# Optimization experiments

Hardware: AMD Instinct MI355X
Metric: run time of the kernel (lower is better)

The kernel has to match this reference:

```python
import jax, jax.numpy as jnp
import numpy as np

XZ = jnp.array([0, 2])
XY = jnp.array([0, 1])
YZ = jnp.array([1, 2])


def _bilinear(plane, uv):
    """plane: (C,R,R) as (C,H,W); uv: (N,2) in [0,1], uv[:,0]->width, uv[:,1]->height.
    Border padding + align_corners=True semantics (grid_sample style)."""
    R = plane.shape[-1]
    xy = jnp.clip(uv, 0.0, 1.0) * (R - 1)
    x, y = xy[:, 0], xy[:, 1]
    x0 = jnp.floor(x)
    y0 = jnp.floor(y)
    x0i = jnp.clip(x0.astype(jnp.int32), 0, R - 1)
    y0i = jnp.clip(y0.astype(jnp.int32), 0, R - 1)
    x1i = jnp.clip(x0i + 1, 0, R - 1)
    y1i = jnp.clip(y0i + 1, 0, R - 1)
    wx = (x - x0)[None, :]  # (1,N)
    wy = (y - y0)[None, :]
    f00 = plane[:, y0i, x0i]  # (C,N)
    f01 = plane[:, y0i, x1i]
    f10 = plane[:, y1i, x0i]
    f11 = plane[:, y1i, x1i]
    top = f00 * (1.0 - wx) + f01 * wx
    bot = f10 * (1.0 - wx) + f11 * wx
    return (top * (1.0 - wy) + bot * wy).T  # (N,C)


def _sample_triplane(p, c_xz, c_xy, c_yz):
    """p: (bs,N,3) in [0,1]; planes: (bs,C,R,R). Returns (bs,N,C) summed over planes."""
    def per_batch(pb, fxz, fxy, fyz):
        return (_bilinear(fxz, pb[:, XZ])
                + _bilinear(fxy, pb[:, XY])
                + _bilinear(fyz, pb[:, YZ]))
    return jax.vmap(per_batch)(p, c_xz, c_xy, c_yz)


def setup_inputs() -> dict:
    key = jax.random.key(0)
    ks = jax.random.split(key, 12)
    bs, ns, C, S, R = 2, 50000, 32, 8, 128
    inp = {
        "query_pos": jax.random.uniform(ks[0], (bs, ns, 3), dtype=jnp.float32),
        "c_xz": jax.random.normal(ks[1], (bs, C, R, R), dtype=jnp.float32),
        "c_xy": jax.random.normal(ks[2], (bs, C, R, R), dtype=jnp.float32),
        "c_yz": jax.random.normal(ks[3], (bs, C, R, R), dtype=jnp.float32),
        # offset weights scaled small so sampled points stay mostly in-bounds
        "W_off": jax.random.normal(ks[4], (C, S * 3), dtype=jnp.float32) * 0.01,
        "b_off": jnp.zeros((S * 3,), dtype=jnp.float32),
        "W_w": jax.random.normal(ks[5], (C, S), dtype=jnp.float32) * 0.1,
        "b_w": jnp.zeros((S,), dtype=jnp.float32),
        "W_v": jax.random.normal(ks[6], (C, C), dtype=jnp.float32) * (1.0 / np.sqrt(C)),
        "b_v": jnp.zeros((C,), dtype=jnp.float32),
        "W_out": jax.random.normal(ks[7], (C, C), dtype=jnp.float32) * (1.0 / np.sqrt(C)),
        "b_out": jnp.zeros((C,), dtype=jnp.float32),
    }
    return inp


def reference(query_pos, c_xz, c_xy, c_yz, W_off, b_off, W_w, b_w, W_v, b_v, W_out, b_out):
    bs, ns, _ = query_pos.shape
    S = W_w.shape[1]
    # round 1: sample tri-plane features at query points
    feature = _sample_triplane(query_pos, c_xz, c_xy, c_yz)  # (bs,ns,C)
    # predict per-query sample offsets and weights
    off = (feature @ W_off + b_off).reshape(bs, ns, S, 3)
    w = (feature @ W_w + b_w).reshape(bs, ns, S, 1)
    pts = off + query_pos[:, :, None, :]  # (bs,ns,S,3)
    # round 2: sample at deformed points
    aux = _sample_triplane(pts.reshape(bs, ns * S, 3), c_xz, c_xy, c_yz)
    v = aux.reshape(bs, ns, S, -1) @ W_v + b_v  # (bs,ns,S,C)
    out = (v * w).sum(-2)                        # weighted reduce over samples
    out = out @ W_out + b_out + feature          # residual
    return out  # (bs,ns,C)
```

## Files before the change

kernel.cpp:

```cpp
#include <hip/hip_runtime.h>
#include <hip/hip_fp16.h>

#define BS 2
#define NS 50000
#define CCH 32
#define RR 128
#define SS 8

typedef float v2f __attribute__((ext_vector_type(2)));
typedef _Float16 h2 __attribute__((ext_vector_type(2)));

#if __has_builtin(__builtin_amdgcn_fdot2)
#define HAVE_DOT2 1
#else
#define HAVE_DOT2 0
#endif


__device__ __forceinline__ unsigned pk_rn(float a, float b) {
    unsigned h0 = __half_as_ushort(__float2half(a));
    unsigned h1 = __half_as_ushort(__float2half(b));
    return h0 | (h1 << 16);
}

__global__ __launch_bounds__(256)
void prep(const float* __restrict__ cxz,
          const float* __restrict__ cxy,
          const float* __restrict__ cyz,
          const float* __restrict__ Wv, const float* __restrict__ bv,
          const float* __restrict__ Wout,
          unsigned* __restrict__ tp, float* __restrict__ Wc,
          float* __restrict__ bvw) {
    __shared__ float lds[32 * 129];
    int tid = threadIdx.x;
    int row = blockIdx.x;
    if (row < BS * 3 * RR) {
        int y  = row & 127;
        int pl = (row >> 7) % 3;
        int b  = row / 384;
        const float* src = (pl == 0) ? cxz : ((pl == 1) ? cxy : cyz);
        const float* sp = src + (((size_t)(b * CCH)) << 14) + (y << 7);
        int c = tid >> 3, xq = tid & 7;
        const float4* s4 = (const float4*)(sp + ((size_t)c << 14));
#pragma unroll
        for (int k = 0; k < 4; ++k) {
            float4 v = s4[xq + 8 * k];
            int x = (xq + 8 * k) << 2;
            lds[c * 129 + x + 0] = v.x;
            lds[c * 129 + x + 1] = v.y;
            lds[c * 129 + x + 2] = v.z;
            lds[c * 129 + x + 3] = v.w;
        }
        __syncthreads();
        uint4* dst = (uint4*)(tp + ((size_t)row << 12));
#pragma unroll
        for (int i = 0; i < 4; ++i) {
            int j = tid + 256 * i;
            int x  = j >> 3;
            int c0 = (j & 7) << 2;
            int x1 = min(x + 1, 127);
            uint4 o;
            o.x = pk_rn(lds[(c0 + 0) * 129 + x], lds[(c0 + 0) * 129 + x1]);
            o.y = pk_rn(lds[(c0 + 1) * 129 + x], lds[(c0 + 1) * 129 + x1]);
            o.z = pk_rn(lds[(c0 + 2) * 129 + x], lds[(c0 + 2) * 129 + x1]);
            o.w = pk_rn(lds[(c0 + 3) * 129 + x], lds[(c0 + 3) * 129 + x1]);
            dst[j] = o;
        }
    } else {
        int t = (row - BS * 3 * RR) * 256 + tid;
        int c = t >> 5, j = t & 31;
        float acc = 0.f;
#pragma unroll
        for (int k = 0; k < 32; ++k) acc += Wv[c * 32 + k] * Wout[k * 32 + j];
        Wc[t] = acc;
        if (t < 32) {
            float a2 = 0.f;
#pragma unroll
            for (int k = 0; k < 32; ++k) a2 += bv[k] * Wout[k * 32 + t];
            bvw[t] = a2;
        }
    }
}


struct f4 { v2f lo, hi; };

struct Coord {
    int o0, o1, o2, o3, o4, o5;
    float wc0, wc1, wr1, wr2;
};

__device__ __forceinline__ Coord coord(float p0, float p1, float p2) {
    Coord c;
    float x0c = fminf(fmaxf(p0, 0.f), 1.f) * 127.f;
    int i0 = min((int)x0c, 126);
    c.wc0 = x0c - (float)i0;
    float x1c = fminf(fmaxf(p1, 0.f), 1.f) * 127.f;
    int i1 = min((int)x1c, 126);
    c.wc1 = x1c - (float)i1;
    float f1 = floorf(x1c);
    int r10 = (int)f1, r11 = min(r10 + 1, 127);
    c.wr1 = x1c - f1;
    float x2c = fminf(fmaxf(p2, 0.f), 1.f) * 127.f;
    float f2 = floorf(x2c);
    int r20 = (int)f2, r21 = min(r20 + 1, 127);
    c.wr2 = x2c - f2;
    int c0 = i0 << 7, c1 = i1 << 7;
    c.o0 = (r20 << 14) + c0;
    c.o1 = (r21 << 14) + c0;
    c.o2 = (1 << 21) + (r10 << 14) + c0;
    c.o3 = (1 << 21) + (r11 << 14) + c0;
    c.o4 = (2 << 21) + (r20 << 14) + c1;
    c.o5 = (2 << 21) + (r21 << 14) + c1;
    return c;
}

__device__ __forceinline__ uint4 ldtap(const char* __restrict__ tpb, int off) {
    return *(const uint4*)(tpb + off);
}

struct SampB { uint4 u[6]; };

__device__ __forceinline__ unsigned pack2(float a, float b) {
#if HAVE_DOT2
    return __builtin_bit_cast(unsigned, __builtin_amdgcn_cvt_pkrtz(a, b));
#else
    __half2 h = __floats2half2_rn(a, b);
    return __builtin_bit_cast(unsigned, h);
#endif
}

#if HAVE_DOT2
__device__ __forceinline__ void eval_row(f4& acc, uint4 u, h2 w) {
    acc.lo.x = __builtin_amdgcn_fdot2(__builtin_bit_cast(h2, u.x), w, acc.lo.x, false);
    acc.lo.y = __builtin_amdgcn_fdot2(__builtin_bit_cast(h2, u.y), w, acc.lo.y, false);
    acc.hi.x = __builtin_amdgcn_fdot2(__builtin_bit_cast(h2, u.z), w, acc.hi.x, false);
    acc.hi.y = __builtin_amdgcn_fdot2(__builtin_bit_cast(h2, u.w), w, acc.hi.y, false);
}

__device__ __forceinline__ void eval_plane(f4& acc, uint4 ua, uint4 ub,
                                           float wx, float wy) {
    float wB1 = wx * wy;
    float wB0 = wx - wB1;
    float wA1 = wy - wB1;
    float wA0 = 1.f - wx - wA1;
    h2 w0 = __builtin_bit_cast(h2, __builtin_amdgcn_cvt_pkrtz(wA0, wB0));
    h2 w1 = __builtin_bit_cast(h2, __builtin_amdgcn_cvt_pkrtz(wA1, wB1));
    eval_row(acc, ua, w0);
    eval_row(acc, ub, w1);
}

__device__ __forceinline__ void eval_rowp(f4& acc, uint4 u, unsigned pw) {
    eval_row(acc, u, __builtin_bit_cast(h2, pw));
}

__device__ __forceinline__ void dot2_4(f4& acc, uint4 wv, unsigned pw) {
    h2 w = __builtin_bit_cast(h2, pw);
    acc.lo.x = __builtin_amdgcn_fdot2(__builtin_bit_cast(h2, wv.x), w, acc.lo.x, false);
    acc.lo.y = __builtin_amdgcn_fdot2(__builtin_bit_cast(h2, wv.y), w, acc.lo.y, false);
    acc.hi.x = __builtin_amdgcn_fdot2(__builtin_bit_cast(h2, wv.z), w, acc.hi.x, false);
    acc.hi.y = __builtin_amdgcn_fdot2(__builtin_bit_cast(h2, wv.w), w, acc.hi.y, false);
}
#else
__device__ __forceinline__ void eval_row(f4& acc, uint4 u, float wA, float wB) {
    __half2 h0 = __builtin_bit_cast(__half2, u.x);
    __half2 h1 = __builtin_bit_cast(__half2, u.y);
    __half2 h2_ = __builtin_bit_cast(__half2, u.z);
    __half2 h3 = __builtin_bit_cast(__half2, u.w);
    acc.lo.x = fmaf(__half2float(h0.y), wB, fmaf(__half2float(h0.x), wA, acc.lo.x));
    acc.lo.y = fmaf(__half2float(h1.y), wB, fmaf(__half2float(h1.x), wA, acc.lo.y));
    acc.hi.x = fmaf(__half2float(h2_.y), wB, fmaf(__half2float(h2_.x), wA, acc.hi.x));
    acc.hi.y = fmaf(__half2float(h3.y), wB, fmaf(__half2float(h3.x), wA, acc.hi.y));
}

__device__ __forceinline__ void eval_plane(f4& acc, uint4 ua, uint4 ub,
                                           float wx, float wy) {
    float wB1 = wx * wy;
    float wB0 = wx - wB1;
    float wA1 = wy - wB1;
    float wA0 = 1.f - wx - wA1;
    eval_row(acc, ua, wA0, wB0);
    eval_row(acc, ub, wA1, wB1);
}

__device__ __forceinline__ void eval_rowp(f4& acc, uint4 u, unsigned pw) {
    __half2 hw = __builtin_bit_cast(__half2, pw);
    eval_row(acc, u, __half2float(hw.x), __half2float(hw.y));
}

__device__ __forceinline__ void dot2_4(f4& acc, uint4 wv, unsigned pw) {
    __half2 hw = __builtin_bit_cast(__half2, pw);
    float a0 = __half2float(hw.x), a1 = __half2float(hw.y);
    __half2 w0 = __builtin_bit_cast(__half2, wv.x);
    __half2 w1 = __builtin_bit_cast(__half2, wv.y);
    __half2 w2_ = __builtin_bit_cast(__half2, wv.z);
    __half2 w3 = __builtin_bit_cast(__half2, wv.w);
    acc.lo.x = fmaf(__half2float(w0.y), a1, fmaf(__half2float(w0.x), a0, acc.lo.x));
    acc.lo.y = fmaf(__half2float(w1.y), a1, fmaf(__half2float(w1.x), a0, acc.lo.y));
    acc.hi.x = fmaf(__half2float(w2_.y), a1, fmaf(__half2float(w2_.x), a0, acc.hi.x));
    acc.hi.y = fmaf(__half2float(w3.y), a1, fmaf(__half2float(w3.x), a0, acc.hi.y));
}
#endif

#define GETE(v, idx) (((idx) & 2) ? (((idx) & 1) ? (v).hi.y : (v).hi.x) \
                                  : (((idx) & 1) ? (v).lo.y : (v).lo.x))
#define GETC(v, idx) __shfl(GETE(v, idx), base | ((idx) >> 2), 64)

__global__ __launch_bounds__(256)
void eda_main(const float* __restrict__ qp, const unsigned* __restrict__ tp,
              const float* __restrict__ Woff, const float* __restrict__ boff,
              const float* __restrict__ Ww, const float* __restrict__ bw,
              const float* __restrict__ Wc, const float* __restrict__ bvw,
              const float* __restrict__ bout, float* __restrict__ out) {
    __shared__ float    sWcat[32][32];
    __shared__ unsigned sWc2h[16][32];
    __shared__ float sbcat[32];
    __shared__ float sbvw[32];
    __shared__ float sbout[32];

    int tid = threadIdx.x;
    int lane = tid & 7;
    int lane16 = lane << 4;
    int base = tid & 56;
    int b  = blockIdx.x & 1;
    int qi = (blockIdx.x >> 1) * 32 + (tid >> 3);
    int qq = min(qi, NS - 1);

    const float* p = qp + ((size_t)b * NS + qq) * 3;
    float p0 = p[0], p1 = p[1], p2 = p[2];

    const char* tpb = (const char*)tp + ((size_t)(b * 3) << 21);

    Coord fc = coord(p0, p1, p2);
    SampB fs;
    fs.u[0] = ldtap(tpb, fc.o0 + lane16); fs.u[1] = ldtap(tpb, fc.o1 + lane16);
    fs.u[2] = ldtap(tpb, fc.o2 + lane16); fs.u[3] = ldtap(tpb, fc.o3 + lane16);
    fs.u[4] = ldtap(tpb, fc.o4 + lane16); fs.u[5] = ldtap(tpb, fc.o5 + lane16);

    for (int i = tid; i < 1024; i += 256) {
        int k = i >> 5, j = i & 31, l2 = j >> 2, e = j & 3;
        sWcat[k][j] = (e < 3) ? Woff[k * 24 + 3 * l2 + e] : Ww[k * 8 + l2];
    }
    {
        int k2 = tid >> 5, j = tid & 31;
        sWc2h[k2][j]     = pk_rn(Wc[k2 * 64 + j],        Wc[k2 * 64 + 32 + j]);
        sWc2h[k2 + 8][j] = pk_rn(Wc[(k2 + 8) * 64 + j],  Wc[(k2 + 8) * 64 + 32 + j]);
    }
    if (tid < 32) {
        int l2 = tid >> 2, e = tid & 3;
        sbcat[tid] = (e < 3) ? boff[3 * l2 + e] : bw[l2];
        sbvw[tid]  = bvw[tid];
        sbout[tid] = bout[tid];
    }
    __syncthreads();

    f4 feat; feat.lo = (v2f){0.f, 0.f}; feat.hi = (v2f){0.f, 0.f};
    eval_plane(feat, fs.u[0], fs.u[1], fc.wc0, fc.wr2);
    eval_plane(feat, fs.u[2], fs.u[3], fc.wc0, fc.wr1);
    eval_plane(feat, fs.u[4], fs.u[5], fc.wc1, fc.wr2);

    f4 cat;
    cat.lo.x = sbcat[(lane << 2) + 0]; cat.lo.y = sbcat[(lane << 2) + 1];
    cat.hi.x = sbcat[(lane << 2) + 2]; cat.hi.y = sbcat[(lane << 2) + 3];
#pragma unroll
    for (int k = 0; k < 32; ++k) {
        float fcv = GETC(feat, k);
        const v2f* wp = (const v2f*)&sWcat[k][lane << 2];
        v2f fc2 = {fcv, fcv};
        cat.lo = __builtin_elementwise_fma(fc2, wp[0], cat.lo);
        cat.hi = __builtin_elementwise_fma(fc2, wp[1], cat.hi);
    }

    Coord my = coord(p0 + cat.lo.x, p1 + cat.lo.y, p2 + cat.hi.x);
    float wt_my = cat.hi.y;
    unsigned m0, m1, m2, m3, m4, m5;
    { float wB1 = my.wc0 * my.wr2, wB0 = my.wc0 - wB1, wA1 = my.wr2 - wB1, wA0 = 1.f - my.wc0 - wA1;
      m0 = pack2(wA0 * wt_my, wB0 * wt_my); m1 = pack2(wA1 * wt_my, wB1 * wt_my); }
    { float wB1 = my.wc0 * my.wr1, wB0 = my.wc0 - wB1, wA1 = my.wr1 - wB1, wA0 = 1.f - my.wc0 - wA1;
      m2 = pack2(wA0 * wt_my, wB0 * wt_my); m3 = pack2(wA1 * wt_my, wB1 * wt_my); }
    { float wB1 = my.wc1 * my.wr2, wB0 = my.wc1 - wB1, wA1 = my.wr2 - wB1, wA0 = 1.f - my.wc1 - wA1;
      m4 = pack2(wA0 * wt_my, wB0 * wt_my); m5 = pack2(wA1 * wt_my, wB1 * wt_my); }

    float wsum = wt_my;
    wsum += __shfl_xor(wsum, 1, 64);
    wsum += __shfl_xor(wsum, 2, 64);
    wsum += __shfl_xor(wsum, 4, 64);

    f4 wa; wa.lo = (v2f){0.f, 0.f}; wa.hi = (v2f){0.f, 0.f};
    SampB cur, nxt;
    {
        int src = base;
        cur.u[0] = ldtap(tpb, __shfl(my.o0, src, 64) + lane16);
        cur.u[1] = ldtap(tpb, __shfl(my.o1, src, 64) + lane16);
        cur.u[2] = ldtap(tpb, __shfl(my.o2, src, 64) + lane16);
        cur.u[3] = ldtap(tpb, __shfl(my.o3, src, 64) + lane16);
        cur.u[4] = ldtap(tpb, __shfl(my.o4, src, 64) + lane16);
        cur.u[5] = ldtap(tpb, __shfl(my.o5, src, 64) + lane16);
    }
#pragma unroll
    for (int s = 0; s < SS; ++s) {
        if (s < SS - 1) {
            int src = base | (s + 1);
            nxt.u[0] = ldtap(tpb, __shfl(my.o0, src, 64) + lane16);
            nxt.u[1] = ldtap(tpb, __shfl(my.o1, src, 64) + lane16);
            nxt.u[2] = ldtap(tpb, __shfl(my.o2, src, 64) + lane16);
            nxt.u[3] = ldtap(tpb, __shfl(my.o3, src, 64) + lane16);
            nxt.u[4] = ldtap(tpb, __shfl(my.o4, src, 64) + lane16);
            nxt.u[5] = ldtap(tpb, __shfl(my.o5, src, 64) + lane16);
        }
        int src = base | s;
        eval_rowp(wa, cur.u[0], (unsigned)__shfl((int)m0, src, 64));
        eval_rowp(wa, cur.u[1], (unsigned)__shfl((int)m1, src, 64));
        eval_rowp(wa, cur.u[2], (unsigned)__shfl((int)m2, src, 64));
        eval_rowp(wa, cur.u[3], (unsigned)__shfl((int)m3, src, 64));
        eval_rowp(wa, cur.u[4], (unsigned)__shfl((int)m4, src, 64));
        eval_rowp(wa, cur.u[5], (unsigned)__shfl((int)m5, src, 64));
        if (s < SS - 1) cur = nxt;
    }

    f4 o;
    v2f ws2 = {wsum, wsum};
    {
        v2f bo  = {sbout[(lane << 2) + 0], sbout[(lane << 2) + 1]};
        v2f bv2 = {sbvw[(lane << 2) + 0], sbvw[(lane << 2) + 1]};
        o.lo = __builtin_elementwise_fma(ws2, bv2, bo) + feat.lo;
        v2f bo2 = {sbout[(lane << 2) + 2], sbout[(lane << 2) + 3]};
        v2f bv3 = {sbvw[(lane << 2) + 2], sbvw[(lane << 2) + 3]};
        o.hi = __builtin_elementwise_fma(ws2, bv3, bo2) + feat.hi;
    }
    unsigned pkLo = pack2(wa.lo.x, wa.lo.y);
    unsigned pkHi = pack2(wa.hi.x, wa.hi.y);
#pragma unroll
    for (int k2 = 0; k2 < 16; ++k2) {
        unsigned wb = (unsigned)__shfl((int)((k2 & 1) ? pkHi : pkLo), base | (k2 >> 1), 64);
        const uint4 wv = *(const uint4*)&sWc2h[k2][lane << 2];
        dot2_4(o, wv, wb);
    }

    if (qi < NS) {
        float* dst = out + ((size_t)b * NS + qi) * 32 + (lane << 2);
        *(float4*)dst = make_float4(o.lo.x, o.lo.y, o.hi.x, o.hi.y);
    }
}

extern "C" void kernel_launch(void* const* d_in, const int* in_sizes, int n_in,
                              void* d_out, int out_size, void* d_ws, size_t ws_size,
                              hipStream_t stream) {
    const float* qp   = (const float*)d_in[0];
    const float* cxz  = (const float*)d_in[1];
    const float* cxy  = (const float*)d_in[2];
    const float* cyz  = (const float*)d_in[3];
    const float* Woff = (const float*)d_in[4];
    const float* boff = (const float*)d_in[5];
    const float* Ww   = (const float*)d_in[6];
    const float* bw   = (const float*)d_in[7];
    const float* Wv   = (const float*)d_in[8];
    const float* bv   = (const float*)d_in[9];
    const float* Wout = (const float*)d_in[10];
    const float* bout = (const float*)d_in[11];
    float* out = (float*)d_out;

    unsigned* tp = (unsigned*)d_ws;
    float* Wc  = (float*)((char*)d_ws + (size_t)BS * 3 * RR * RR * CCH * 4);
    float* bvw = Wc + 1024;

    prep<<<BS * 3 * RR + 4, 256, 0, stream>>>(cxz, cxy, cyz, Wv, bv, Wout, tp, Wc, bvw);
    int blocks_per_batch = (NS + 31) / 32;
    eda_main<<<2 * blocks_per_batch, 256, 0, stream>>>(qp, tp, Woff, boff, Ww, bw,
                                                       Wc, bvw, bout, out);
}
```

Measured before the change: 129.9 us.

## Process two query groups per thread to raise memory-level parallelism

Each block now handles 64 queries instead of 32, with every thread interleaving two independent queries (A and B) through all stages: first-round tap loads, offset/weight projection, pipelined second-round gathers and the output projection. The aim is more outstanding gathers per wave, shared-memory weight loads reused across two queries, and setup cost amortised over half as many blocks. It roughly doubles live registers, which can lower occupancy or cause spills, and halves the grid size.

```diff
diff --git a/kernel.cpp b/kernel.cpp
--- a/kernel.cpp
+++ b/kernel.cpp
@@ -206,6 +206,14 @@
                                   : (((idx) & 1) ? (v).lo.y : (v).lo.x))
 #define GETC(v, idx) __shfl(GETE(v, idx), base | ((idx) >> 2), 64)
 
+struct Q {
+    float p0, p1, p2;
+    f4 feat, cat, wa;
+    Coord my;
+    unsigned m0, m1, m2, m3, m4, m5;
+    float wsum;
+};
+
 __global__ __launch_bounds__(256)
 void eda_main(const float* __restrict__ qp, const unsigned* __restrict__ tp,
               const float* __restrict__ Woff, const float* __restrict__ boff,
@@ -223,19 +231,28 @@
     int lane16 = lane << 4;
     int base = tid & 56;
     int b  = blockIdx.x & 1;
-    int qi = (blockIdx.x >> 1) * 32 + (tid >> 3);
-    int qq = min(qi, NS - 1);
-
-    const float* p = qp + ((size_t)b * NS + qq) * 3;
-    float p0 = p[0], p1 = p[1], p2 = p[2];
+    int qiA = (blockIdx.x >> 1) * 64 + (tid >> 3);
+    int qiB = qiA + 32;
+    int qqA = min(qiA, NS - 1);
+    int qqB = min(qiB, NS - 1);
+
+    const float* pA = qp + ((size_t)b * NS + qqA) * 3;
+    const float* pB = qp + ((size_t)b * NS + qqB) * 3;
+    Q A, B;
+    A.p0 = pA[0]; A.p1 = pA[1]; A.p2 = pA[2];
+    B.p0 = pB[0]; B.p1 = pB[1]; B.p2 = pB[2];
 
     const char* tpb = (const char*)tp + ((size_t)(b * 3) << 21);
 
-    Coord fc = coord(p0, p1, p2);
-    SampB fs;
-    fs.u[0] = ldtap(tpb, fc.o0 + lane16); fs.u[1] = ldtap(tpb, fc.o1 + lane16);
-    fs.u[2] = ldtap(tpb, fc.o2 + lane16); fs.u[3] = ldtap(tpb, fc.o3 + lane16);
-    fs.u[4] = ldtap(tpb, fc.o4 + lane16); fs.u[5] = ldtap(tpb, fc.o5 + lane16);
+    Coord fcA = coord(A.p0, A.p1, A.p2);
+    Coord fcB = coord(B.p0, B.p1, B.p2);
+    SampB fsA, fsB;
+    fsA.u[0] = ldtap(tpb, fcA.o0 + lane16); fsA.u[1] = ldtap(tpb, fcA.o1 + lane16);
+    fsA.u[2] = ldtap(tpb, fcA.o2 + lane16); fsA.u[3] = ldtap(tpb, fcA.o3 + lane16);
+    fsA.u[4] = ldtap(tpb, fcA.o4 + lane16); fsA.u[5] = ldtap(tpb, fcA.o5 + lane16);
+    fsB.u[0] = ldtap(tpb, fcB.o0 + lane16); fsB.u[1] = ldtap(tpb, fcB.o1 + lane16);
+    fsB.u[2] = ldtap(tpb, fcB.o2 + lane16); fsB.u[3] = ldtap(tpb, fcB.o3 + lane16);
+    fsB.u[4] = ldtap(tpb, fcB.o4 + lane16); fsB.u[5] = ldtap(tpb, fcB.o5 + lane16);
 
     for (int i = tid; i < 1024; i += 256) {
         int k = i >> 5, j = i & 31, l2 = j >> 2, e = j & 3;
@@ -254,92 +271,146 @@
     }
     __syncthreads();
 
-    f4 feat; feat.lo = (v2f){0.f, 0.f}; feat.hi = (v2f){0.f, 0.f};
-    eval_plane(feat, fs.u[0], fs.u[1], fc.wc0, fc.wr2);
-    eval_plane(feat, fs.u[2], fs.u[3], fc.wc0, fc.wr1);
-    eval_plane(feat, fs.u[4], fs.u[5], fc.wc1, fc.wr2);
-
-    f4 cat;
-    cat.lo.x = sbcat[(lane << 2) + 0]; cat.lo.y = sbcat[(lane << 2) + 1];
-    cat.hi.x = sbcat[(lane << 2) + 2]; cat.hi.y = sbcat[(lane << 2) + 3];
+    A.feat.lo = (v2f){0.f, 0.f}; A.feat.hi = (v2f){0.f, 0.f};
+    eval_plane(A.feat, fsA.u[0], fsA.u[1], fcA.wc0, fcA.wr2);
+    eval_plane(A.feat, fsA.u[2], fsA.u[3], fcA.wc0, fcA.wr1);
+    eval_plane(A.feat, fsA.u[4], fsA.u[5], fcA.wc1, fcA.wr2);
+    B.feat.lo = (v2f){0.f, 0.f}; B.feat.hi = (v2f){0.f, 0.f};
+    eval_plane(B.feat, fsB.u[0], fsB.u[1], fcB.wc0, fcB.wr2);
+    eval_plane(B.feat, fsB.u[2], fsB.u[3], fcB.wc0, fcB.wr1);
+    eval_plane(B.feat, fsB.u[4], fsB.u[5], fcB.wc1, fcB.wr2);
+
+    A.cat.lo.x = sbcat[(lane << 2) + 0]; A.cat.lo.y = sbcat[(lane << 2) + 1];
+    A.cat.hi.x = sbcat[(lane << 2) + 2]; A.cat.hi.y = sbcat[(lane << 2) + 3];
+    B.cat = A.cat;
 #pragma unroll
     for (int k = 0; k < 32; ++k) {
-        float fcv = GETC(feat, k);
+        float fA = GETC(A.feat, k);
+        float fB = GETC(B.feat, k);
         const v2f* wp = (const v2f*)&sWcat[k][lane << 2];
-        v2f fc2 = {fcv, fcv};
-        cat.lo = __builtin_elementwise_fma(fc2, wp[0], cat.lo);
-        cat.hi = __builtin_elementwise_fma(fc2, wp[1], cat.hi);
-    }
-
-    Coord my = coord(p0 + cat.lo.x, p1 + cat.lo.y, p2 + cat.hi.x);
-    float wt_my = cat.hi.y;
-    unsigned m0, m1, m2, m3, m4, m5;
-    { float wB1 = my.wc0 * my.wr2, wB0 = my.wc0 - wB1, wA1 = my.wr2 - wB1, wA0 = 1.f - my.wc0 - wA1;
-      m0 = pack2(wA0 * wt_my, wB0 * wt_my); m1 = pack2(wA1 * wt_my, wB1 * wt_my); }
-    { float wB1 = my.wc0 * my.wr1, wB0 = my.wc0 - wB1, wA1 = my.wr1 - wB1, wA0 = 1.f - my.wc0 - wA1;
-      m2 = pack2(wA0 * wt_my, wB0 * wt_my); m3 = pack2(wA1 * wt_my, wB1 * wt_my); }
-    { float wB1 = my.wc1 * my.wr2, wB0 = my.wc1 - wB1, wA1 = my.wr2 - wB1, wA0 = 1.f - my.wc1 - wA1;
-      m4 = pack2(wA0 * wt_my, wB0 * wt_my); m5 = pack2(wA1 * wt_my, wB1 * wt_my); }
-
-    float wsum = wt_my;
-    wsum += __shfl_xor(wsum, 1, 64);
-    wsum += __shfl_xor(wsum, 2, 64);
-    wsum += __shfl_xor(wsum, 4, 64);
-
-    f4 wa; wa.lo = (v2f){0.f, 0.f}; wa.hi = (v2f){0.f, 0.f};
-    SampB cur, nxt;
+        v2f w0 = wp[0], w1 = wp[1];
+        v2f fa2 = {fA, fA};
+        v2f fb2 = {fB, fB};
+        A.cat.lo = __builtin_elementwise_fma(fa2, w0, A.cat.lo);
+        A.cat.hi = __builtin_elementwise_fma(fa2, w1, A.cat.hi);
+        B.cat.lo = __builtin_elementwise_fma(fb2, w0, B.cat.lo);
+        B.cat.hi = __builtin_elementwise_fma(fb2, w1, B.cat.hi);
+    }
+
+    A.my = coord(A.p0 + A.cat.lo.x, A.p1 + A.cat.lo.y, A.p2 + A.cat.hi.x);
+    B.my = coord(B.p0 + B.cat.lo.x, B.p1 + B.cat.lo.y, B.p2 + B.cat.hi.x);
+    {
+        float wt = A.cat.hi.y;
+        { float wB1 = A.my.wc0 * A.my.wr2, wB0 = A.my.wc0 - wB1, wA1 = A.my.wr2 - wB1, wA0 = 1.f - A.my.wc0 - wA1;
+          A.m0 = pack2(wA0 * wt, wB0 * wt); A.m1 = pack2(wA1 * wt, wB1 * wt); }
+        { float wB1 = A.my.wc0 * A.my.wr1, wB0 = A.my.wc0 - wB1, wA1 = A.my.wr1 - wB1, wA0 = 1.f - A.my.wc0 - wA1;
+          A.m2 = pack2(wA0 * wt, wB0 * wt); A.m3 = pack2(wA1 * wt, wB1 * wt); }
+        { float wB1 = A.my.wc1 * A.my.wr2, wB0 = A.my.wc1 - wB1, wA1 = A.my.wr2 - wB1, wA0 = 1.f - A.my.wc1 - wA1;
+          A.m4 = pack2(wA0 * wt, wB0 * wt); A.m5 = pack2(wA1 * wt, wB1 * wt); }
+        A.wsum = wt;
+        A.wsum += __shfl_xor(A.wsum, 1, 64);
+        A.wsum += __shfl_xor(A.wsum, 2, 64);
+        A.wsum += __shfl_xor(A.wsum, 4, 64);
+    }
+    {
+        float wt = B.cat.hi.y;
+        { float wB1 = B.my.wc0 * B.my.wr2, wB0 = B.my.wc0 - wB1, wA1 = B.my.wr2 - wB1, wA0 = 1.f - B.my.wc0 - wA1;
+          B.m0 = pack2(wA0 * wt, wB0 * wt); B.m1 = pack2(wA1 * wt, wB1 * wt); }
+        { float wB1 = B.my.wc0 * B.my.wr1, wB0 = B.my.wc0 - wB1, wA1 = B.my.wr1 - wB1, wA0 = 1.f - B.my.wc0 - wA1;
+          B.m2 = pack2(wA0 * wt, wB0 * wt); B.m3 = pack2(wA1 * wt, wB1 * wt); }
+        { float wB1 = B.my.wc1 * B.my.wr2, wB0 = B.my.wc1 - wB1, wA1 = B.my.wr2 - wB1, wA0 = 1.f - B.my.wc1 - wA1;
+          B.m4 = pack2(wA0 * wt, wB0 * wt); B.m5 = pack2(wA1 * wt, wB1 * wt); }
+        B.wsum = wt;
+        B.wsum += __shfl_xor(B.wsum, 1, 64);
+        B.wsum += __shfl_xor(B.wsum, 2, 64);
+        B.wsum += __shfl_xor(B.wsum, 4, 64);
+    }
+
+    A.wa.lo = (v2f){0.f, 0.f}; A.wa.hi = (v2f){0.f, 0.f};
+    B.wa = A.wa;
+    SampB curA, curB, nxtA, nxtB;
     {
         int src = base;
-        cur.u[0] = ldtap(tpb, __shfl(my.o0, src, 64) + lane16);
-        cur.u[1] = ldtap(tpb, __shfl(my.o1, src, 64) + lane16);
-        cur.u[2] = ldtap(tpb, __shfl(my.o2, src, 64) + lane16);
-        cur.u[3] = ldtap(tpb, __shfl(my.o3, src, 64) + lane16);
-        cur.u[4] = ldtap(tpb, __shfl(my.o4, src, 64) + lane16);
-        cur.u[5] = ldtap(tpb, __shfl(my.o5, src, 64) + lane16);
+        curA.u[0] = ldtap(tpb, __shfl(A.my.o0, src, 64) + lane16);
+        curA.u[1] = ldtap(tpb, __shfl(A.my.o1, src, 64) + lane16);
+        curA.u[2] = ldtap(tpb, __shfl(A.my.o2, src, 64) + lane16);
+        curA.u[3] = ldtap(tpb, __shfl(A.my.o3, src, 64) + lane16);
+        curA.u[4] = ldtap(tpb, __shfl(A.my.o4, src, 64) + lane16);
+        curA.u[5] = ldtap(tpb, __shfl(A.my.o5, src, 64) + lane16);
+        curB.u[0] = ldtap(tpb, __shfl(B.my.o0, src, 64) + lane16);
+        curB.u[1] = ldtap(tpb, __shfl(B.my.o1, src, 64) + lane16);
+        curB.u[2] = ldtap(tpb, __shfl(B.my.o2, src, 64) + lane16);
+        curB.u[3] = ldtap(tpb, __shfl(B.my.o3, src, 64) + lane16);
+        curB.u[4] = ldtap(tpb, __shfl(B.my.o4, src, 64) + lane16);
+        curB.u[5] = ldtap(tpb, __shfl(B.my.o5, src, 64) + lane16);
     }
 #pragma unroll
     for (int s = 0; s < SS; ++s) {
         if (s < SS - 1) {
             int src = base | (s + 1);
-            nxt.u[0] = ldtap(tpb, __shfl(my.o0, src, 64) + lane16);
-            nxt.u[1] = ldtap(tpb, __shfl(my.o1, src, 64) + lane16);
-            nxt.u[2] = ldtap(tpb, __shfl(my.o2, src, 64) + lane16);
-            nxt.u[3] = ldtap(tpb, __shfl(my.o3, src, 64) + lane16);
-            nxt.u[4] = ldtap(tpb, __shfl(my.o4, src, 64) + lane16);
-            nxt.u[5] = ldtap(tpb, __shfl(my.o5, src, 64) + lane16);
+            nxtA.u[0] = ldtap(tpb, __shfl(A.my.o0, src, 64) + lane16);
+            nxtA.u[1] = ldtap(tpb, __shfl(A.my.o1, src, 64) + lane16);
+            nxtA.u[2] = ldtap(tpb, __shfl(A.my.o2, src, 64) + lane16);
+            nxtA.u[3] = ldtap(tpb, __shfl(A.my.o3, src, 64) + lane16);
+            nxtA.u[4] = ldtap(tpb, __shfl(A.my.o4, src, 64) + lane16);
+            nxtA.u[5] = ldtap(tpb, __shfl(A.my.o5, src, 64) + lane16);
+            nxtB.u[0] = ldtap(tpb, __shfl(B.my.o0, src, 64) + lane16);
+            nxtB.u[1] = ldtap(tpb, __shfl(B.my.o1, src, 64) + lane16);
+            nxtB.u[2] = ldtap(tpb, __shfl(B.my.o2, src, 64) + lane16);
+            nxtB.u[3] = ldtap(tpb, __shfl(B.my.o3, src, 64) + lane16);
+            nxtB.u[4] = ldtap(tpb, __shfl(B.my.o4, src, 64) + lane16);
+            nxtB.u[5] = ldtap(tpb, __shfl(B.my.o5, src, 64) + lane16);
         }
         int src = base | s;
-        eval_rowp(wa, cur.u[0], (unsigned)__shfl((int)m0, src, 64));
-        eval_rowp(wa, cur.u[1], (unsigned)__shfl((int)m1, src, 64));
-        eval_rowp(wa, cur.u[2], (unsigned)__shfl((int)m2, src, 64));
-        eval_rowp(wa, cur.u[3], (unsigned)__shfl((int)m3, src, 64));
-        eval_rowp(wa, cur.u[4], (unsigned)__shfl((int)m4, src, 64));
-        eval_rowp(wa, cur.u[5], (unsigned)__shfl((int)m5, src, 64));
-        if (s < SS - 1) cur = nxt;
-    }
-
-    f4 o;
-    v2f ws2 = {wsum, wsum};
+        eval_rowp(A.wa, curA.u[0], (unsigned)__shfl((int)A.m0, src, 64));
+        eval_rowp(A.wa, curA.u[1], (unsigned)__shfl((int)A.m1, src, 64));
+        eval_rowp(A.wa, curA.u[2], (unsigned)__shfl((int)A.m2, src, 64));
+        eval_rowp(A.wa, curA.u[3], (unsigned)__shfl((int)A.m3, src, 64));
+        eval_rowp(A.wa, curA.u[4], (unsigned)__shfl((int)A.m4, src, 64));
+        eval_rowp(A.wa, curA.u[5], (unsigned)__shfl((int)A.m5, src, 64));
+        eval_rowp(B.wa, curB.u[0], (unsigned)__shfl((int)B.m0, src, 64));
+        eval_rowp(B.wa, curB.u[1], (unsigned)__shfl((int)B.m1, src, 64));
+        eval_rowp(B.wa, curB.u[2], (unsigned)__shfl((int)B.m2, src, 64));
+        eval_rowp(B.wa, curB.u[3], (unsigned)__shfl((int)B.m3, src, 64));
+        eval_rowp(B.wa, curB.u[4], (unsigned)__shfl((int)B.m4, src, 64));
+        eval_rowp(B.wa, curB.u[5], (unsigned)__shfl((int)B.m5, src, 64));
+        if (s < SS - 1) { curA = nxtA; curB = nxtB; }
+    }
+
+    f4 oA, oB;
     {
         v2f bo  = {sbout[(lane << 2) + 0], sbout[(lane << 2) + 1]};
+        v2f bo2 = {sbout[(lane << 2) + 2], sbout[(lane << 2) + 3]};
         v2f bv2 = {sbvw[(lane << 2) + 0], sbvw[(lane << 2) + 1]};
-        o.lo = __builtin_elementwise_fma(ws2, bv2, bo) + feat.lo;
-        v2f bo2 = {sbout[(lane << 2) + 2], sbout[(lane << 2) + 3]};
         v2f bv3 = {sbvw[(lane << 2) + 2], sbvw[(lane << 2) + 3]};
-        o.hi = __builtin_elementwise_fma(ws2, bv3, bo2) + feat.hi;
-    }
-    unsigned pkLo = pack2(wa.lo.x, wa.lo.y);
-    unsigned pkHi = pack2(wa.hi.x, wa.hi.y);
+        v2f wsA = {A.wsum, A.wsum};
+        v2f wsB = {B.wsum, B.wsum};
+        oA.lo = __builtin_elementwise_fma(wsA, bv2, bo)  + A.feat.lo;
+        oA.hi = __builtin_elementwise_fma(wsA, bv3, bo2) + A.feat.hi;
+        oB.lo = __builtin_elementwise_fma(wsB, bv2, bo)  + B.feat.lo;
+        oB.hi = __builtin_elementwise_fma(wsB, bv3, bo2) + B.feat.hi;
+    }
+    unsigned pkLoA = pack2(A.wa.lo.x, A.wa.lo.y);
+    unsigned pkHiA = pack2(A.wa.hi.x, A.wa.hi.y);
+    unsigned pkLoB = pack2(B.wa.lo.x, B.wa.lo.y);
+    unsigned pkHiB = pack2(B.wa.hi.x, B.wa.hi.y);
 #pragma unroll
     for (int k2 = 0; k2 < 16; ++k2) {
-        unsigned wb = (unsigned)__shfl((int)((k2 & 1) ? pkHi : pkLo), base | (k2 >> 1), 64);
+        int src = base | (k2 >> 1);
+        unsigned wbA = (unsigned)__shfl((int)((k2 & 1) ? pkHiA : pkLoA), src, 64);
+        unsigned wbB = (unsigned)__shfl((int)((k2 & 1) ? pkHiB : pkLoB), src, 64);
         const uint4 wv = *(const uint4*)&sWc2h[k2][lane << 2];
-        dot2_4(o, wv, wb);
-    }
-
-    if (qi < NS) {
-        float* dst = out + ((size_t)b * NS + qi) * 32 + (lane << 2);
-        *(float4*)dst = make_float4(o.lo.x, o.lo.y, o.hi.x, o.hi.y);
+        dot2_4(oA, wv, wbA);
+        dot2_4(oB, wv, wbB);
+    }
+
+    if (qiA < NS) {
+        float* dst = out + ((size_t)b * NS + qiA) * 32 + (lane << 2);
+        *(float4*)dst = make_float4(oA.lo.x, oA.lo.y, oA.hi.x, oA.hi.y);
+    }
+    if (qiB < NS) {
+        float* dst = out + ((size_t)b * NS + qiB) * 32 + (lane << 2);
+        *(float4*)dst = make_float4(oB.lo.x, oB.lo.y, oB.hi.x, oB.hi.y);
     }
 }
 
@@ -365,7 +436,7 @@
     float* bvw = Wc + 1024;
 
     prep<<<BS * 3 * RR + 4, 256, 0, stream>>>(cxz, cxy, cyz, Wv, bv, Wout, tp, Wc, bvw);
-    int blocks_per_batch = (NS + 31) / 32;
+    int blocks_per_batch = (NS + 63) / 64;
     eda_main<<<2 * blocks_per_batch, 256, 0, stream>>>(qp, tp, Woff, boff, Ww, bw,
                                                        Wc, bvw, bout, out);
 }
```

New measurement: 136.3 us. +4.9%, slower.
